# Kernel tuning notes

Measured on AMD Instinct MI355X. Metric: run time of the kernel, lower is better.

The kernel has to match this reference:

```python
import jax, jax.numpy as jnp
import numpy as np

HEADS = 32
DK = 32            # att_size = hidden // heads
CUT = 15.5         # tot_dis[cur_layer=0] + 0.5
NEG = -1e8
LN_EPS = 1e-5


def layernorm(x, g, b):
    m = jnp.mean(x, axis=-1, keepdims=True)
    v = jnp.mean((x - m) ** 2, axis=-1, keepdims=True)
    return (x - m) / jnp.sqrt(v + LN_EPS) * g + b


def setup_inputs() -> dict:
    key = jax.random.key(0)
    ks = jax.random.split(key, 12)
    B, S, H, F = 8, 513, 1024, 4096
    N = S - 1
    def nrm(k, shape, scale=0.02):
        return jax.random.normal(k, shape, jnp.float32) * scale
    x = jax.random.normal(ks[0], (B, S, H), jnp.float32)
    attn_bias = jax.random.normal(ks[1], (B, HEADS, S, S), jnp.float32)
    rel_pos = jax.random.randint(ks[2], (B, N, N), 0, 16, jnp.int32)
    rel_emb = nrm(ks[3], (512, HEADS)).at[0].set(0.0)  # padding_idx=0
    Wq = nrm(ks[4], (H, H)); bq = jnp.zeros((H,), jnp.float32)
    Wk = nrm(ks[5], (H, H)); bk = jnp.zeros((H,), jnp.float32)
    Wv = nrm(ks[6], (H, H)); bv = jnp.zeros((H,), jnp.float32)
    Wo = nrm(ks[7], (H, H)); bo = jnp.zeros((H,), jnp.float32)
    W1 = nrm(ks[8], (H, F)); b1 = jnp.zeros((F,), jnp.float32)
    W2 = nrm(ks[9], (F, H)); b2 = jnp.zeros((H,), jnp.float32)
    ln1_g = jnp.ones((H,), jnp.float32); ln1_b = jnp.zeros((H,), jnp.float32)
    ln2_g = jnp.ones((H,), jnp.float32); ln2_b = jnp.zeros((H,), jnp.float32)
    return dict(x=x, attn_bias=attn_bias, rel_emb=rel_emb,
                Wq=Wq, bq=bq, Wk=Wk, bk=bk, Wv=Wv, bv=bv, Wo=Wo, bo=bo,
                W1=W1, b1=b1, W2=W2, b2=b2,
                ln1_g=ln1_g, ln1_b=ln1_b, ln2_g=ln2_g, ln2_b=ln2_b,
                rel_pos=rel_pos)


def reference(x, attn_bias, rel_emb, Wq, bq, Wk, bk, Wv, bv, Wo, bo,
              W1, b1, W2, b2, ln1_g, ln1_b, ln2_g, ln2_b, rel_pos):
    B, S, H = x.shape
    # rel-pos bias: embed [B,N,N] -> [B,N,N,heads] -> [B,heads,N,N]
    rpb = jnp.transpose(rel_emb[rel_pos], (0, 3, 1, 2))
    inner = attn_bias[:, :, 1:, 1:] + rpb
    # per-head mask flag: keep if within cutoff distance OR already -inf-masked
    flags = (rel_pos[:, None, :, :] <= CUT) | (inner < NEG)
    ab = attn_bias.at[:, :, 1:, 1:].set(inner * flags)
    # attention
    y = layernorm(x, ln1_g, ln1_b)
    scale = DK ** -0.5
    q = (y @ Wq + bq).reshape(B, S, HEADS, DK) * scale
    k = (y @ Wk + bk).reshape(B, S, HEADS, DK)
    v = (y @ Wv + bv).reshape(B, S, HEADS, DK)
    scores = jnp.einsum('bqhd,bkhd->bhqk', q, k) + ab
    attn = jax.nn.softmax(scores, axis=-1)
    o = jnp.einsum('bhqk,bkhd->bqhd', attn, v).reshape(B, S, H)
    x = x + (o @ Wo + bo)
    # FFN
    y = layernorm(x, ln2_g, ln2_b)
    y = jax.nn.gelu(y @ W1 + b1, approximate=False) @ W2 + b2
    return x + y
```

## Files before the change

kernel.cpp:

```cpp
#include <hip/hip_runtime.h>
#include <hip/hip_bf16.h>
#include <math.h>

typedef __attribute__((ext_vector_type(8))) short short8;
typedef __attribute__((ext_vector_type(4))) float f32x4;
typedef unsigned short u16;
typedef unsigned int u32;

#define SQ 513
#define MPAD 4224
#define MV 4104
#define NHEADS 32
#define DKH 32
#define SVP 576

static __device__ inline u16 f2bf(float f) {
  u32 u = __builtin_bit_cast(u32, f);
  u = (u + 0x7fffu + ((u >> 16) & 1u)) >> 16;
  return (u16)u;
}

static __device__ inline void gld16(const void* g, void* l) {
  __builtin_amdgcn_global_load_lds((__attribute__((address_space(1))) void*)g,
                                   (__attribute__((address_space(3))) void*)l,
                                   16, 0, 0);
}

static __device__ inline float gelu_f(float x) {
  return 0.5f * x * (1.f + erff(x * 0.70710678118654752f));
}

__global__ __launch_bounds__(256) void transpose_cast_k(const float* __restrict__ in,
    u16* __restrict__ out, int K, int N, float scale)
{
  __shared__ float t[32][33];
  int n0 = blockIdx.x * 32, k0 = blockIdx.y * 32;
  int tx = threadIdx.x & 31, ty = threadIdx.x >> 5;
#pragma unroll
  for (int i = 0; i < 32; i += 8)
    t[ty + i][tx] = in[(size_t)(k0 + ty + i) * N + n0 + tx];
  __syncthreads();
#pragma unroll
  for (int i = 0; i < 32; i += 8)
    out[(size_t)(n0 + ty + i) * K + k0 + tx] = f2bf(t[tx][ty + i] * scale);
}

__global__ __launch_bounds__(256) void vtrans_k(const u16* __restrict__ qkv,
    u16* __restrict__ vT)
{
  __shared__ u16 t[32][33];
  int st = blockIdx.x * 32, h = blockIdx.y, b = blockIdx.z;
  int tx = threadIdx.x & 31, ty = threadIdx.x >> 5;
#pragma unroll
  for (int i = 0; i < 32; i += 8) {
    int s = st + ty + i;
    int sc = s > 512 ? 512 : s;
    t[ty + i][tx] = qkv[(size_t)(b * SQ + sc) * 3072 + 2048 + h * DKH + tx];
  }
  __syncthreads();
#pragma unroll
  for (int i = 0; i < 32; i += 8) {
    int d = ty + i;
    vT[(((size_t)b * NHEADS + h) * DKH + d) * SVP + st + tx] = t[tx][d];
  }
}

__global__ __launch_bounds__(256) void prep_bias_k(const float* __restrict__ bq,
    const float* __restrict__ bk, const float* __restrict__ bv,
    float* __restrict__ out, float scale)
{
  int i = blockIdx.x * 256 + threadIdx.x;
  float v = (i < 1024) ? bq[i] * scale : ((i < 2048) ? bk[i - 1024] : bv[i - 2048]);
  out[i] = v;
}

__global__ __launch_bounds__(256) void ln_k(const float* __restrict__ in,
    const float* __restrict__ g, const float* __restrict__ b,
    u16* __restrict__ out)
{
  int row = blockIdx.x;
  float4 v = ((const float4*)(in + (size_t)row * 1024))[threadIdx.x];
  float s = v.x + v.y + v.z + v.w;
  float s2 = v.x * v.x + v.y * v.y + v.z * v.z + v.w * v.w;
#pragma unroll
  for (int d = 32; d; d >>= 1) { s += __shfl_xor(s, d, 64); s2 += __shfl_xor(s2, d, 64); }
  __shared__ float ps[4], ps2[4];
  int w = threadIdx.x >> 6;
  if ((threadIdx.x & 63) == 0) { ps[w] = s; ps2[w] = s2; }
  __syncthreads();
  s = ps[0] + ps[1] + ps[2] + ps[3];
  s2 = ps2[0] + ps2[1] + ps2[2] + ps2[3];
  float mean = s * (1.f / 1024.f);
  float var = s2 * (1.f / 1024.f) - mean * mean;
  float inv = rsqrtf(var + 1e-5f);
  float4 gv = ((const float4*)g)[threadIdx.x];
  float4 bv = ((const float4*)b)[threadIdx.x];
  ushort4 o;
  o.x = f2bf((v.x - mean) * inv * gv.x + bv.x);
  o.y = f2bf((v.y - mean) * inv * gv.y + bv.y);
  o.z = f2bf((v.z - mean) * inv * gv.z + bv.z);
  o.w = f2bf((v.w - mean) * inv * gv.w + bv.w);
  ((ushort4*)(out + (size_t)row * 1024))[threadIdx.x] = o;
}

template <int EPI>
__global__ __launch_bounds__(256) void gemm_bt(const u16* __restrict__ A,
    const u16* __restrict__ Bw, const float* __restrict__ bias,
    const float* __restrict__ resid, void* __restrict__ outp,
    int N, int K, int nbx)
{
  __shared__ alignas(16) u16 sA[128 * 64];
  __shared__ alignas(16) u16 sB[128 * 64];
  int tid = threadIdx.x;
  int l = tid & 63, lg = l >> 4, li = l & 15;
  int mb = blockIdx.x / nbx, nb = blockIdx.x % nbx;
  int m0 = mb * 128, n0 = nb * 128;
  int wv = tid >> 6;
  int wr = wv >> 1, wc = wv & 1;
  f32x4 acc[4][4] = {};
  int r_ = tid >> 3, c_ = (tid & 7) * 8;
  const u16* Ag = A + (size_t)(m0 + r_) * K + c_;
  const u16* Bg = Bw + (size_t)(n0 + r_) * K + c_;
  u16* sAb = sA + (tid & 192) * 8;
  u16* sBb = sB + (tid & 192) * 8;

  for (int k0 = 0; k0 < K; k0 += 64) {
    __syncthreads();
#pragma unroll
    for (int i = 0; i < 4; ++i) {
      gld16(Ag + (size_t)(i * 32) * K + k0, sAb + i * 2048);
      gld16(Bg + (size_t)(i * 32) * K + k0, sBb + i * 2048);
    }
    __syncthreads();
#pragma unroll
    for (int ks = 0; ks < 2; ++ks) {
      short8 af[4], bfr[4];
#pragma unroll
      for (int i = 0; i < 4; ++i)
        af[i] = *(const short8*)&sA[(64 * wr + 16 * i + li) * 64 + ks * 32 + lg * 8];
#pragma unroll
      for (int j = 0; j < 4; ++j)
        bfr[j] = *(const short8*)&sB[(64 * wc + 16 * j + li) * 64 + ks * 32 + lg * 8];
#pragma unroll
      for (int i = 0; i < 4; ++i)
#pragma unroll
        for (int j = 0; j < 4; ++j)
          acc[i][j] = __builtin_amdgcn_mfma_f32_16x16x32_bf16(af[i], bfr[j], acc[i][j], 0, 0, 0);
    }
  }

#pragma unroll
  for (int i = 0; i < 4; ++i) {
    int rb = m0 + 64 * wr + 16 * i + 4 * lg;
#pragma unroll
    for (int j = 0; j < 4; ++j) {
      int col = n0 + 64 * wc + 16 * j + li;
      float bia = bias[col];
#pragma unroll
      for (int r = 0; r < 4; ++r) {
        int row = rb + r;
        float v = acc[i][j][r] + bia;
        if (EPI == 0) {
          ((u16*)outp)[(size_t)row * N + col] = f2bf(v);
        } else if (EPI == 1) {
          if (row < MV) {
            v += resid[(size_t)row * N + col];
            ((float*)outp)[(size_t)row * N + col] = v;
          }
        } else if (EPI == 2) {
          ((u16*)outp)[(size_t)row * N + col] = f2bf(gelu_f(v));
        } else {
          if (row < MV) ((float*)outp)[(size_t)row * N + col] += v;
        }
      }
    }
  }
}

__global__ __launch_bounds__(256) void attn_fused(const u16* __restrict__ qkv,
    const u16* __restrict__ vT, const float* __restrict__ attn_bias,
    const int* __restrict__ rel_pos, const float* __restrict__ rel_emb,
    u16* __restrict__ o)
{
  __shared__ alignas(16) u16 k_lds[2][64 * 32];
  __shared__ alignas(16) u16 v_lds[2][32 * 64];
  __shared__ alignas(16) u16 p_lds[4][16][72];
  int bid = blockIdx.x;
  int qt = bid % 9, h = (bid / 9) % NHEADS, b = bid / (9 * NHEADS);
  int tid = threadIdx.x, wv = tid >> 6, l = tid & 63, lg = l >> 4, li = l & 15;
  int q0 = qt * 64;
  int sqb = q0 + 16 * wv + 4 * lg;

  short8 qfrag = *(const short8*)(qkv + (size_t)(b * SQ + q0 + 16 * wv + li) * 3072 + h * DKH + lg * 8);

  float tv = rel_emb[(size_t)li * NHEADS + h];

  const float* bias_row[4];
  const int* rp_row[4];
#pragma unroll
  for (int r = 0; r < 4; ++r) {
    int sq = sqb + r;
    int sqc = sq > 512 ? 512 : sq;
    bias_row[r] = attn_bias + (((size_t)b * NHEADS + h) * SQ + sqc) * SQ;
    int sqm = sq - 1; sqm = sqm < 0 ? 0 : (sqm > 511 ? 511 : sqm);
    rp_row[r] = rel_pos + ((size_t)b * 512 + sqm) * 512;
  }

  int krow = tid >> 2;
  int kchunk = (tid & 3) ^ ((tid >> 3) & 3);
  const u16* ksrc = qkv + (size_t)(b * SQ) * 3072 + 1024 + h * DKH + kchunk * 8;
  int vrow = tid >> 3;
  int vchunk = (tid & 7) ^ (vrow & 7);
  const u16* vsrc = vT + (((size_t)b * NHEADS + h) * DKH + vrow) * SVP + vchunk * 8;

  int koff[4], voff[4];
#pragma unroll
  for (int f = 0; f < 4; ++f)
    koff[f] = (16 * f + li) * 32 + ((lg ^ ((li >> 1) & 3)) * 8);
#pragma unroll
  for (int u = 0; u < 4; ++u) {
    int df = u >> 1, kk = u & 1;
    voff[u] = (16 * df + li) * 64 + (((kk * 4 + lg) ^ (li & 7)) * 8);
  }

  float pb[4][4];
  int pr[4][4];

  gld16(ksrc + (size_t)krow * 3072, (u16*)k_lds[0] + tid * 8);
  gld16(vsrc, (u16*)v_lds[0] + tid * 8);
#pragma unroll
  for (int f = 0; f < 4; ++f) {
    int sk = 16 * f + li;
    int skm = sk - 1; skm = skm < 0 ? 0 : skm;
#pragma unroll
    for (int r = 0; r < 4; ++r) {
      pb[f][r] = bias_row[r][sk];
      pr[f][r] = rp_row[r][skm];
    }
  }

  f32x4 o_acc[2] = {};
  float m_run[4], l_run[4];
#pragma unroll
  for (int r = 0; r < 4; ++r) { m_run[r] = -1e30f; l_run[r] = 0.f; }

  for (int kt = 0; kt < 9; ++kt) {
    int cur = kt & 1;
    __syncthreads();
    if (kt < 8) {
      int s = (kt + 1) * 64 + krow; if (s > 512) s = 512;
      gld16(ksrc + (size_t)s * 3072, (u16*)k_lds[cur ^ 1] + tid * 8);
      gld16(vsrc + (size_t)(kt + 1) * 64, (u16*)v_lds[cur ^ 1] + tid * 8);
    }
    const u16* kb = k_lds[cur];
    const u16* vbf = v_lds[cur];

    f32x4 sc[4];
#pragma unroll
    for (int f = 0; f < 4; ++f) {
      short8 kf = *(const short8*)&kb[koff[f]];
      f32x4 z = {};
      sc[f] = __builtin_amdgcn_mfma_f32_16x16x32_bf16(qfrag, kf, z, 0, 0, 0);
    }

#pragma unroll
    for (int f = 0; f < 4; ++f) {
      int sk = kt * 64 + 16 * f + li;
#pragma unroll
      for (int r = 0; r < 4; ++r) {
        int sq = sqb + r;
        float base = pb[f][r];
        int rp = pr[f][r];
        float re = __shfl(tv, rp, 64);
        float inner = base + re;
        float ab = (rp <= 15 || inner < -1e8f) ? inner : 0.f;
        if (sq == 0 || sk == 0) ab = base;
        if (sq > 512 || sk > 512) ab = -1e30f;
        sc[f][r] += ab;
      }
    }
    if (kt < 8) {
#pragma unroll
      for (int f = 0; f < 4; ++f) {
        int sk = (kt + 1) * 64 + 16 * f + li;
        int skc = sk > 512 ? 512 : sk;
        int skm = sk - 1; skm = skm > 511 ? 511 : skm;
#pragma unroll
        for (int r = 0; r < 4; ++r) {
          pb[f][r] = bias_row[r][skc];
          pr[f][r] = rp_row[r][skm];
        }
      }
    }

    float alpha[4];
#pragma unroll
    for (int r = 0; r < 4; ++r) {
      float mx = fmaxf(fmaxf(sc[0][r], sc[1][r]), fmaxf(sc[2][r], sc[3][r]));
#pragma unroll
      for (int d = 1; d < 16; d <<= 1) mx = fmaxf(mx, __shfl_xor(mx, d, 16));
      float mn = fmaxf(m_run[r], mx);
      alpha[r] = __expf(m_run[r] - mn);
      m_run[r] = mn;
      l_run[r] *= alpha[r];
    }
#pragma unroll
    for (int f = 0; f < 4; ++f)
#pragma unroll
      for (int r = 0; r < 4; ++r) {
        float p = __expf(sc[f][r] - m_run[r]);
        l_run[r] += p;
        p_lds[wv][4 * lg + r][16 * f + li] = f2bf(p);
      }
#pragma unroll
    for (int df = 0; df < 2; ++df)
#pragma unroll
      for (int r = 0; r < 4; ++r) o_acc[df][r] *= alpha[r];

#pragma unroll
    for (int kk = 0; kk < 2; ++kk) {
      short8 pa = *(const short8*)&p_lds[wv][li][kk * 32 + lg * 8];
#pragma unroll
      for (int df = 0; df < 2; ++df) {
        short8 vb = *(const short8*)&vbf[voff[df * 2 + kk]];
        o_acc[df] = __builtin_amdgcn_mfma_f32_16x16x32_bf16(pa, vb, o_acc[df], 0, 0, 0);
      }
    }
  }

#pragma unroll
  for (int r = 0; r < 4; ++r) {
    float s = l_run[r];
#pragma unroll
    for (int d = 1; d < 16; d <<= 1) s += __shfl_xor(s, d, 16);
    l_run[r] = s;
  }
#pragma unroll
  for (int df = 0; df < 2; ++df)
#pragma unroll
    for (int r = 0; r < 4; ++r) {
      int s_q = sqb + r;
      if (s_q <= 512)
        o[(size_t)(b * SQ + s_q) * 1024 + h * DKH + 16 * df + li] = f2bf(o_acc[df][r] / l_run[r]);
    }
}

extern "C" void kernel_launch(void* const* d_in, const int* in_sizes, int n_in,
                              void* d_out, int out_size, void* d_ws, size_t ws_size,
                              hipStream_t stream) {
  const float* x        = (const float*)d_in[0];
  const float* attn_bias= (const float*)d_in[1];
  const float* rel_emb  = (const float*)d_in[2];
  const float* Wq = (const float*)d_in[3];
  const float* bq = (const float*)d_in[4];
  const float* Wk = (const float*)d_in[5];
  const float* bk = (const float*)d_in[6];
  const float* Wv = (const float*)d_in[7];
  const float* bv = (const float*)d_in[8];
  const float* Wo = (const float*)d_in[9];
  const float* bo = (const float*)d_in[10];
  const float* W1 = (const float*)d_in[11];
  const float* b1 = (const float*)d_in[12];
  const float* W2 = (const float*)d_in[13];
  const float* b2 = (const float*)d_in[14];
  const float* ln1g = (const float*)d_in[15];
  const float* ln1b = (const float*)d_in[16];
  const float* ln2g = (const float*)d_in[17];
  const float* ln2b = (const float*)d_in[18];
  const int*   rel_pos = (const int*)d_in[19];
  float* out = (float*)d_out;

  char* ws = (char*)d_ws;
  size_t off = 0;
  auto alloc = [&](size_t bytes) { char* p = ws + off; off += (bytes + 255) & ~(size_t)255; return p; };
  u16* w_qkvT = (u16*)alloc((size_t)3072 * 1024 * 2);
  u16* w_oT   = (u16*)alloc((size_t)1024 * 1024 * 2);
  u16* w_1T   = (u16*)alloc((size_t)4096 * 1024 * 2);
  u16* w_2T   = (u16*)alloc((size_t)1024 * 4096 * 2);
  float* bias_qkv = (float*)alloc(3072 * 4);
  u16* ybuf = (u16*)alloc((size_t)MPAD * 1024 * 2);
  u16* obuf = (u16*)alloc((size_t)MPAD * 1024 * 2);
  u16* vTb  = (u16*)alloc((size_t)8 * NHEADS * DKH * SVP * 2);
  u16* big  = (u16*)alloc((size_t)MPAD * 4096 * 2);

  const float scale = 0.17677669529663689f;
  dim3 blk(256);

  transpose_cast_k<<<dim3(32, 32), blk, 0, stream>>>(Wq, w_qkvT, 1024, 1024, scale);
  transpose_cast_k<<<dim3(32, 32), blk, 0, stream>>>(Wk, w_qkvT + (size_t)1024 * 1024, 1024, 1024, 1.f);
  transpose_cast_k<<<dim3(32, 32), blk, 0, stream>>>(Wv, w_qkvT + (size_t)2048 * 1024, 1024, 1024, 1.f);
  transpose_cast_k<<<dim3(32, 32), blk, 0, stream>>>(Wo, w_oT, 1024, 1024, 1.f);
  transpose_cast_k<<<dim3(128, 32), blk, 0, stream>>>(W1, w_1T, 1024, 4096, 1.f);
  transpose_cast_k<<<dim3(32, 128), blk, 0, stream>>>(W2, w_2T, 4096, 1024, 1.f);
  prep_bias_k<<<12, blk, 0, stream>>>(bq, bk, bv, bias_qkv, scale);

  ln_k<<<MV, blk, 0, stream>>>(x, ln1g, ln1b, ybuf);
  gemm_bt<0><<<33 * 24, blk, 0, stream>>>(ybuf, w_qkvT, bias_qkv, nullptr, big, 3072, 1024, 24);
  vtrans_k<<<dim3(18, NHEADS, 8), blk, 0, stream>>>(big, vTb);
  attn_fused<<<8 * NHEADS * 9, blk, 0, stream>>>(big, vTb, attn_bias, rel_pos, rel_emb, obuf);
  gemm_bt<1><<<33 * 8, blk, 0, stream>>>(obuf, w_oT, bo, x, out, 1024, 1024, 8);
  ln_k<<<MV, blk, 0, stream>>>(out, ln2g, ln2b, ybuf);
  gemm_bt<2><<<33 * 32, blk, 0, stream>>>(ybuf, w_1T, b1, nullptr, big, 4096, 1024, 32);
  gemm_bt<3><<<33 * 8, blk, 0, stream>>>(big, w_2T, b2, nullptr, out, 1024, 4096, 8);
}
```

Before: 499.4 us.

## Split-K the FFN2 GEMM and widen attention KV tiles to 128

The FFN2 GEMM is split into two K-halves, each writing a float partial buffer, and a separate combine kernel adds both partials, the bias and the residual. This doubles the block count so the 264-block GEMM fills the GPU better. Separately, the attention kernel now processes 128 keys per iteration instead of 64 (5 iterations rather than 9), with a re-swizzled LDS layout, a larger V transpose padding, and launch bounds asking for 3 blocks per CU. The trade-offs are extra partial-buffer traffic plus one more kernel launch, and higher register and LDS pressure in attention.

```diff
diff --git a/kernel.cpp b/kernel.cpp
--- a/kernel.cpp
+++ b/kernel.cpp
@@ -12,7 +12,8 @@
 #define MV 4104
 #define NHEADS 32
 #define DKH 32
-#define SVP 576
+#define SVP 640
+#define KVB 128
 
 static __device__ inline u16 f2bf(float f) {
   u32 u = __builtin_bit_cast(u32, f);
@@ -113,7 +114,19 @@
   __shared__ alignas(16) u16 sB[128 * 64];
   int tid = threadIdx.x;
   int l = tid & 63, lg = l >> 4, li = l & 15;
-  int mb = blockIdx.x / nbx, nb = blockIdx.x % nbx;
+
+  int bidx = blockIdx.x;
+  int kbeg = 0, kend = K;
+  float* pout = (float*)outp;
+  if (EPI == 4) {
+    int half = gridDim.x >> 1;
+    int s = bidx >= half;
+    bidx -= s * half;
+    kbeg = s * (K >> 1);
+    kend = kbeg + (K >> 1);
+    pout += (size_t)s * MPAD * 1024;
+  }
+  int mb = bidx / nbx, nb = bidx % nbx;
   int m0 = mb * 128, n0 = nb * 128;
   int wv = tid >> 6;
   int wr = wv >> 1, wc = wv & 1;
@@ -124,7 +137,7 @@
   u16* sAb = sA + (tid & 192) * 8;
   u16* sBb = sB + (tid & 192) * 8;
 
-  for (int k0 = 0; k0 < K; k0 += 64) {
+  for (int k0 = kbeg; k0 < kend; k0 += 64) {
     __syncthreads();
 #pragma unroll
     for (int i = 0; i < 4; ++i) {
@@ -155,7 +168,7 @@
 #pragma unroll
     for (int j = 0; j < 4; ++j) {
       int col = n0 + 64 * wc + 16 * j + li;
-      float bia = bias[col];
+      float bia = (EPI == 4) ? 0.f : bias[col];
 #pragma unroll
       for (int r = 0; r < 4; ++r) {
         int row = rb + r;
@@ -170,21 +183,37 @@
         } else if (EPI == 2) {
           ((u16*)outp)[(size_t)row * N + col] = f2bf(gelu_f(v));
         } else {
-          if (row < MV) ((float*)outp)[(size_t)row * N + col] += v;
+          pout[(size_t)row * N + col] = v;
         }
       }
     }
   }
 }
 
-__global__ __launch_bounds__(256) void attn_fused(const u16* __restrict__ qkv,
+__global__ __launch_bounds__(256) void ffn2_combine(const float* __restrict__ part,
+    float* __restrict__ out, const float* __restrict__ b2)
+{
+  size_t idx = (size_t)blockIdx.x * 256 + threadIdx.x;
+  const float4* p0 = (const float4*)part;
+  const float4* p1 = (const float4*)(part + (size_t)MPAD * 1024);
+  float4 a = ((float4*)out)[idx];
+  float4 x0 = p0[idx], x1 = p1[idx];
+  float4 bb = ((const float4*)b2)[idx & 255];
+  a.x += x0.x + x1.x + bb.x;
+  a.y += x0.y + x1.y + bb.y;
+  a.z += x0.z + x1.z + bb.z;
+  a.w += x0.w + x1.w + bb.w;
+  ((float4*)out)[idx] = a;
+}
+
+__global__ __launch_bounds__(256, 3) void attn_fused(const u16* __restrict__ qkv,
     const u16* __restrict__ vT, const float* __restrict__ attn_bias,
     const int* __restrict__ rel_pos, const float* __restrict__ rel_emb,
     u16* __restrict__ o)
 {
-  __shared__ alignas(16) u16 k_lds[2][64 * 32];
-  __shared__ alignas(16) u16 v_lds[2][32 * 64];
-  __shared__ alignas(16) u16 p_lds[4][16][72];
+  __shared__ alignas(16) u16 k_lds[2][KVB * 32];
+  __shared__ alignas(16) u16 v_lds[2][32 * KVB];
+  __shared__ alignas(16) u16 p_lds[4][16][KVB + 8];
   int bid = blockIdx.x;
   int qt = bid % 9, h = (bid / 9) % NHEADS, b = bid / (9 * NHEADS);
   int tid = threadIdx.x, wv = tid >> 6, l = tid & 63, lg = l >> 4, li = l & 15;
@@ -207,29 +236,32 @@
   }
 
   int krow = tid >> 2;
-  int kchunk = (tid & 3) ^ ((tid >> 3) & 3);
+  int kchunk = (tid & 3) ^ ((krow >> 1) & 3);
   const u16* ksrc = qkv + (size_t)(b * SQ) * 3072 + 1024 + h * DKH + kchunk * 8;
-  int vrow = tid >> 3;
-  int vchunk = (tid & 7) ^ (vrow & 7);
-  const u16* vsrc = vT + (((size_t)b * NHEADS + h) * DKH + vrow) * SVP + vchunk * 8;
-
-  int koff[4], voff[4];
-#pragma unroll
-  for (int f = 0; f < 4; ++f)
+  int vrow = tid >> 4;
+  int vchunk = (tid & 15) ^ (vrow & 15);
+  const u16* vsrc = vT + (((size_t)b * NHEADS + h) * DKH) * SVP + vchunk * 8;
+
+  int koff[8];
+#pragma unroll
+  for (int f = 0; f < 8; ++f)
     koff[f] = (16 * f + li) * 32 + ((lg ^ ((li >> 1) & 3)) * 8);
-#pragma unroll
-  for (int u = 0; u < 4; ++u) {
-    int df = u >> 1, kk = u & 1;
-    voff[u] = (16 * df + li) * 64 + (((kk * 4 + lg) ^ (li & 7)) * 8);
-  }
-
-  float pb[4][4];
-  int pr[4][4];
+  int voff[2][4];
+#pragma unroll
+  for (int df = 0; df < 2; ++df)
+#pragma unroll
+    for (int kk = 0; kk < 4; ++kk)
+      voff[df][kk] = (16 * df + li) * KVB + (((kk * 4 + lg) ^ li) * 8);
+
+  float pb[8][4];
+  int pr[8][4];
 
   gld16(ksrc + (size_t)krow * 3072, (u16*)k_lds[0] + tid * 8);
-  gld16(vsrc, (u16*)v_lds[0] + tid * 8);
-#pragma unroll
-  for (int f = 0; f < 4; ++f) {
+  gld16(ksrc + (size_t)(krow + 64) * 3072, (u16*)k_lds[0] + 2048 + tid * 8);
+  gld16(vsrc + (size_t)vrow * SVP, (u16*)v_lds[0] + tid * 8);
+  gld16(vsrc + (size_t)(vrow + 16) * SVP, (u16*)v_lds[0] + 2048 + tid * 8);
+#pragma unroll
+  for (int f = 0; f < 8; ++f) {
     int sk = 16 * f + li;
     int skm = sk - 1; skm = skm < 0 ? 0 : skm;
 #pragma unroll
@@ -244,28 +276,32 @@
 #pragma unroll
   for (int r = 0; r < 4; ++r) { m_run[r] = -1e30f; l_run[r] = 0.f; }
 
-  for (int kt = 0; kt < 9; ++kt) {
+  for (int kt = 0; kt < 5; ++kt) {
     int cur = kt & 1;
     __syncthreads();
-    if (kt < 8) {
-      int s = (kt + 1) * 64 + krow; if (s > 512) s = 512;
-      gld16(ksrc + (size_t)s * 3072, (u16*)k_lds[cur ^ 1] + tid * 8);
-      gld16(vsrc + (size_t)(kt + 1) * 64, (u16*)v_lds[cur ^ 1] + tid * 8);
+    if (kt < 4) {
+      int s0 = (kt + 1) * KVB + krow;       int sa = s0 > 512 ? 512 : s0;
+      int s1 = (kt + 1) * KVB + krow + 64;  int sb = s1 > 512 ? 512 : s1;
+      gld16(ksrc + (size_t)sa * 3072, (u16*)k_lds[cur ^ 1] + tid * 8);
+      gld16(ksrc + (size_t)sb * 3072, (u16*)k_lds[cur ^ 1] + 2048 + tid * 8);
+      const u16* vn = vsrc + (size_t)(kt + 1) * KVB;
+      gld16(vn + (size_t)vrow * SVP, (u16*)v_lds[cur ^ 1] + tid * 8);
+      gld16(vn + (size_t)(vrow + 16) * SVP, (u16*)v_lds[cur ^ 1] + 2048 + tid * 8);
     }
     const u16* kb = k_lds[cur];
     const u16* vbf = v_lds[cur];
 
-    f32x4 sc[4];
-#pragma unroll
-    for (int f = 0; f < 4; ++f) {
+    f32x4 sc[8];
+#pragma unroll
+    for (int f = 0; f < 8; ++f) {
       short8 kf = *(const short8*)&kb[koff[f]];
       f32x4 z = {};
       sc[f] = __builtin_amdgcn_mfma_f32_16x16x32_bf16(qfrag, kf, z, 0, 0, 0);
     }
 
 #pragma unroll
-    for (int f = 0; f < 4; ++f) {
-      int sk = kt * 64 + 16 * f + li;
+    for (int f = 0; f < 8; ++f) {
+      int sk = kt * KVB + 16 * f + li;
 #pragma unroll
       for (int r = 0; r < 4; ++r) {
         int sq = sqb + r;
@@ -279,10 +315,10 @@
         sc[f][r] += ab;
       }
     }
-    if (kt < 8) {
-#pragma unroll
-      for (int f = 0; f < 4; ++f) {
-        int sk = (kt + 1) * 64 + 16 * f + li;
+    if (kt < 4) {
+#pragma unroll
+      for (int f = 0; f < 8; ++f) {
+        int sk = (kt + 1) * KVB + 16 * f + li;
         int skc = sk > 512 ? 512 : sk;
         int skm = sk - 1; skm = skm > 511 ? 511 : skm;
 #pragma unroll
@@ -296,7 +332,9 @@
     float alpha[4];
 #pragma unroll
     for (int r = 0; r < 4; ++r) {
-      float mx = fmaxf(fmaxf(sc[0][r], sc[1][r]), fmaxf(sc[2][r], sc[3][r]));
+      float mx = sc[0][r];
+#pragma unroll
+      for (int f = 1; f < 8; ++f) mx = fmaxf(mx, sc[f][r]);
 #pragma unroll
       for (int d = 1; d < 16; d <<= 1) mx = fmaxf(mx, __shfl_xor(mx, d, 16));
       float mn = fmaxf(m_run[r], mx);
@@ -305,7 +343,7 @@
       l_run[r] *= alpha[r];
     }
 #pragma unroll
-    for (int f = 0; f < 4; ++f)
+    for (int f = 0; f < 8; ++f)
 #pragma unroll
       for (int r = 0; r < 4; ++r) {
         float p = __expf(sc[f][r] - m_run[r]);
@@ -318,11 +356,11 @@
       for (int r = 0; r < 4; ++r) o_acc[df][r] *= alpha[r];
 
 #pragma unroll
-    for (int kk = 0; kk < 2; ++kk) {
+    for (int kk = 0; kk < 4; ++kk) {
       short8 pa = *(const short8*)&p_lds[wv][li][kk * 32 + lg * 8];
 #pragma unroll
       for (int df = 0; df < 2; ++df) {
-        short8 vb = *(const short8*)&vbf[voff[df * 2 + kk]];
+        short8 vb = *(const short8*)&vbf[voff[df][kk]];
         o_acc[df] = __builtin_amdgcn_mfma_f32_16x16x32_bf16(pa, vb, o_acc[df], 0, 0, 0);
       }
     }
@@ -382,6 +420,7 @@
   u16* obuf = (u16*)alloc((size_t)MPAD * 1024 * 2);
   u16* vTb  = (u16*)alloc((size_t)8 * NHEADS * DKH * SVP * 2);
   u16* big  = (u16*)alloc((size_t)MPAD * 4096 * 2);
+  float* part = (float*)alloc((size_t)2 * MPAD * 1024 * 4);
 
   const float scale = 0.17677669529663689f;
   dim3 blk(256);
@@ -396,10 +435,11 @@
 
   ln_k<<<MV, blk, 0, stream>>>(x, ln1g, ln1b, ybuf);
   gemm_bt<0><<<33 * 24, blk, 0, stream>>>(ybuf, w_qkvT, bias_qkv, nullptr, big, 3072, 1024, 24);
-  vtrans_k<<<dim3(18, NHEADS, 8), blk, 0, stream>>>(big, vTb);
+  vtrans_k<<<dim3(20, NHEADS, 8), blk, 0, stream>>>(big, vTb);
   attn_fused<<<8 * NHEADS * 9, blk, 0, stream>>>(big, vTb, attn_bias, rel_pos, rel_emb, obuf);
   gemm_bt<1><<<33 * 8, blk, 0, stream>>>(obuf, w_oT, bo, x, out, 1024, 1024, 8);
   ln_k<<<MV, blk, 0, stream>>>(out, ln2g, ln2b, ybuf);
   gemm_bt<2><<<33 * 32, blk, 0, stream>>>(ybuf, w_1T, b1, nullptr, big, 4096, 1024, 32);
-  gemm_bt<3><<<33 * 8, blk, 0, stream>>>(big, w_2T, b2, nullptr, out, 1024, 4096, 8);
-}
+  gemm_bt<4><<<33 * 8 * 2, blk, 0, stream>>>(big, w_2T, b2, nullptr, part, 1024, 4096, 8);
+  ffn2_combine<<<MV, blk, 0, stream>>>(part, out, b2);
+}
```

After: 898.9 us. 1.8x slower.

## Split-K the FFN2 GEMM and specialize attention tile boundary handling

Applied to the files above, without the earlier changes.

The FFN2 GEMM (K=4096) previously launched only 264 blocks. It now splits K in half, doubling the grid, and writes fp32 partials to a scratch buffer. A new combine kernel sums the two partials with the bias and residual. Separately, the attention loop is specialized into first, middle and last tile variants so the per-element boundary checks and index clamps compile away for interior tiles. The split adds extra fp32 partial traffic and one more kernel launch in exchange for better CU occupancy on the MI355X.

```diff
diff --git a/kernel.cpp b/kernel.cpp
--- a/kernel.cpp
+++ b/kernel.cpp
@@ -1,6 +1,7 @@
 #include <hip/hip_runtime.h>
 #include <hip/hip_bf16.h>
 #include <math.h>
+#include <type_traits>
 
 typedef __attribute__((ext_vector_type(8))) short short8;
 typedef __attribute__((ext_vector_type(4))) float f32x4;
@@ -113,7 +114,19 @@
   __shared__ alignas(16) u16 sB[128 * 64];
   int tid = threadIdx.x;
   int l = tid & 63, lg = l >> 4, li = l & 15;
-  int mb = blockIdx.x / nbx, nb = blockIdx.x % nbx;
+
+  int bidx = blockIdx.x;
+  int kbeg = 0, kend = K;
+  float* pout = (float*)outp;
+  if (EPI == 4) {
+    int half = gridDim.x >> 1;
+    int s = bidx >= half;
+    bidx -= s * half;
+    kbeg = s * (K >> 1);
+    kend = kbeg + (K >> 1);
+    pout += (size_t)s * MPAD * 1024;
+  }
+  int mb = bidx / nbx, nb = bidx % nbx;
   int m0 = mb * 128, n0 = nb * 128;
   int wv = tid >> 6;
   int wr = wv >> 1, wc = wv & 1;
@@ -124,7 +137,7 @@
   u16* sAb = sA + (tid & 192) * 8;
   u16* sBb = sB + (tid & 192) * 8;
 
-  for (int k0 = 0; k0 < K; k0 += 64) {
+  for (int k0 = kbeg; k0 < kend; k0 += 64) {
     __syncthreads();
 #pragma unroll
     for (int i = 0; i < 4; ++i) {
@@ -155,7 +168,7 @@
 #pragma unroll
     for (int j = 0; j < 4; ++j) {
       int col = n0 + 64 * wc + 16 * j + li;
-      float bia = bias[col];
+      float bia = (EPI == 4) ? 0.f : bias[col];
 #pragma unroll
       for (int r = 0; r < 4; ++r) {
         int row = rb + r;
@@ -170,11 +183,27 @@
         } else if (EPI == 2) {
           ((u16*)outp)[(size_t)row * N + col] = f2bf(gelu_f(v));
         } else {
-          if (row < MV) ((float*)outp)[(size_t)row * N + col] += v;
+          pout[(size_t)row * N + col] = v;
         }
       }
     }
   }
+}
+
+__global__ __launch_bounds__(256) void ffn2_combine(const float* __restrict__ part,
+    float* __restrict__ out, const float* __restrict__ b2)
+{
+  size_t idx = (size_t)blockIdx.x * 256 + threadIdx.x;
+  const float4* p0 = (const float4*)part;
+  const float4* p1 = (const float4*)(part + (size_t)MPAD * 1024);
+  float4 a = ((float4*)out)[idx];
+  float4 x0 = p0[idx], x1 = p1[idx];
+  float4 bb = ((const float4*)b2)[idx & 255];
+  a.x += x0.x + x1.x + bb.x;
+  a.y += x0.y + x1.y + bb.y;
+  a.z += x0.z + x1.z + bb.z;
+  a.w += x0.w + x1.w + bb.w;
+  ((float4*)out)[idx] = a;
 }
 
 __global__ __launch_bounds__(256) void attn_fused(const u16* __restrict__ qkv,
@@ -197,9 +226,12 @@
 
   const float* bias_row[4];
   const int* rp_row[4];
+  bool sq_is0[4], sq_hi[4];
 #pragma unroll
   for (int r = 0; r < 4; ++r) {
     int sq = sqb + r;
+    sq_is0[r] = (sq == 0);
+    sq_hi[r] = (sq > 512);
     int sqc = sq > 512 ? 512 : sq;
     bias_row[r] = attn_bias + (((size_t)b * NHEADS + h) * SQ + sqc) * SQ;
     int sqm = sq - 1; sqm = sqm < 0 ? 0 : (sqm > 511 ? 511 : sqm);
@@ -244,10 +276,11 @@
 #pragma unroll
   for (int r = 0; r < 4; ++r) { m_run[r] = -1e30f; l_run[r] = 0.f; }
 
-  for (int kt = 0; kt < 9; ++kt) {
+  auto tile_body = [&](int kt, auto mode_c) {
+    constexpr int MODE = decltype(mode_c)::value;
     int cur = kt & 1;
     __syncthreads();
-    if (kt < 8) {
+    if (MODE != 2) {
       int s = (kt + 1) * 64 + krow; if (s > 512) s = 512;
       gld16(ksrc + (size_t)s * 3072, (u16*)k_lds[cur ^ 1] + tid * 8);
       gld16(vsrc + (size_t)(kt + 1) * 64, (u16*)v_lds[cur ^ 1] + tid * 8);
@@ -265,30 +298,48 @@
 
 #pragma unroll
     for (int f = 0; f < 4; ++f) {
-      int sk = kt * 64 + 16 * f + li;
 #pragma unroll
       for (int r = 0; r < 4; ++r) {
-        int sq = sqb + r;
         float base = pb[f][r];
         int rp = pr[f][r];
         float re = __shfl(tv, rp, 64);
         float inner = base + re;
         float ab = (rp <= 15 || inner < -1e8f) ? inner : 0.f;
-        if (sq == 0 || sk == 0) ab = base;
-        if (sq > 512 || sk > 512) ab = -1e30f;
+        if (MODE == 0) {
+          if (sq_is0[r] || (f == 0 && li == 0)) ab = base;
+          if (sq_hi[r]) ab = -1e30f;
+        } else if (MODE == 1) {
+          if (sq_is0[r]) ab = base;
+          if (sq_hi[r]) ab = -1e30f;
+        } else {
+          if (sq_is0[r]) ab = base;
+          if (sq_hi[r] || (16 * f + li) > 0) ab = -1e30f;
+        }
         sc[f][r] += ab;
       }
     }
-    if (kt < 8) {
-#pragma unroll
-      for (int f = 0; f < 4; ++f) {
-        int sk = (kt + 1) * 64 + 16 * f + li;
-        int skc = sk > 512 ? 512 : sk;
-        int skm = sk - 1; skm = skm > 511 ? 511 : skm;
-#pragma unroll
-        for (int r = 0; r < 4; ++r) {
-          pb[f][r] = bias_row[r][skc];
-          pr[f][r] = rp_row[r][skm];
+
+    if (MODE != 2) {
+      if (kt < 7) {
+        int cb = (kt + 1) * 64 + li;
+#pragma unroll
+        for (int f = 0; f < 4; ++f)
+#pragma unroll
+          for (int r = 0; r < 4; ++r) {
+            pb[f][r] = bias_row[r][cb + 16 * f];
+            pr[f][r] = rp_row[r][cb + 16 * f - 1];
+          }
+      } else {
+#pragma unroll
+        for (int f = 0; f < 4; ++f) {
+          int sk = 512 + 16 * f + li;
+          int skc = sk > 512 ? 512 : sk;
+          int skm = sk - 1; skm = skm > 511 ? 511 : skm;
+#pragma unroll
+          for (int r = 0; r < 4; ++r) {
+            pb[f][r] = bias_row[r][skc];
+            pr[f][r] = rp_row[r][skm];
+          }
         }
       }
     }
@@ -326,7 +377,11 @@
         o_acc[df] = __builtin_amdgcn_mfma_f32_16x16x32_bf16(pa, vb, o_acc[df], 0, 0, 0);
       }
     }
-  }
+  };
+
+  tile_body(0, std::integral_constant<int, 0>{});
+  for (int kt = 1; kt < 8; ++kt) tile_body(kt, std::integral_constant<int, 1>{});
+  tile_body(8, std::integral_constant<int, 2>{});
 
 #pragma unroll
   for (int r = 0; r < 4; ++r) {
@@ -382,6 +437,7 @@
   u16* obuf = (u16*)alloc((size_t)MPAD * 1024 * 2);
   u16* vTb  = (u16*)alloc((size_t)8 * NHEADS * DKH * SVP * 2);
   u16* big  = (u16*)alloc((size_t)MPAD * 4096 * 2);
+  float* part = (float*)alloc((size_t)2 * MPAD * 1024 * 4);
 
   const float scale = 0.17677669529663689f;
   dim3 blk(256);
@@ -401,5 +457,6 @@
   gemm_bt<1><<<33 * 8, blk, 0, stream>>>(obuf, w_oT, bo, x, out, 1024, 1024, 8);
   ln_k<<<MV, blk, 0, stream>>>(out, ln2g, ln2b, ybuf);
   gemm_bt<2><<<33 * 32, blk, 0, stream>>>(ybuf, w_1T, b1, nullptr, big, 4096, 1024, 32);
-  gemm_bt<3><<<33 * 8, blk, 0, stream>>>(big, w_2T, b2, nullptr, out, 1024, 4096, 8);
-}
+  gemm_bt<4><<<33 * 8 * 2, blk, 0, stream>>>(big, w_2T, b2, nullptr, part, 1024, 4096, 8);
+  ffn2_combine<<<MV, blk, 0, stream>>>(part, out, b2);
+}
```

Result: faster. 489.3 us (-2.0%).
